# Kernel optimization log

Hardware: AMD Instinct MI355X
Metric: run time of the kernel (lower is better)

The kernel has to match this reference:

```python
import jax, jax.numpy as jnp
import numpy as np

WINDOW_SIZE = 11
C1 = 0.01 ** 2
C2 = 0.03 ** 2


def _make_window(size: int) -> jnp.ndarray:
    sigma = size / 6.0
    coords = jnp.arange(size, dtype=jnp.float32) - size // 2
    g = jnp.exp(-coords ** 2 / (2 * sigma ** 2))
    g = g / g.sum()
    w = jnp.outer(g, g)
    return w[None, None]  # [1,1,K,K]  (OIHW)


def _conv(x, w, pad):
    # x: [N,1,H,W], w: [1,1,K,K]
    return jax.lax.conv_general_dilated(
        x, w,
        window_strides=(1, 1),
        padding=[(pad, pad), (pad, pad)],
        dimension_numbers=("NCHW", "OIHW", "NCHW"),
    )


def setup_inputs() -> dict:
    key = jax.random.key(0)
    k1, k2 = jax.random.split(key)
    pred = jax.random.uniform(k1, (64, 1, 512, 512), dtype=jnp.float32)
    gt = jax.random.uniform(k2, (64, 1, 512, 512), dtype=jnp.float32)
    return {"pred": pred, "gt": gt}


def reference(pred, gt):
    w = _make_window(WINDOW_SIZE).astype(pred.dtype)
    pad = WINDOW_SIZE // 2
    mu1 = _conv(pred, w, pad)
    mu2 = _conv(gt, w, pad)
    sigma1 = _conv(pred * pred, w, pad) - mu1 ** 2
    sigma2 = _conv(gt * gt, w, pad) - mu2 ** 2
    sigma12 = _conv(pred * gt, w, pad) - mu1 * mu2
    ssim_map = (2 * mu1 * mu2 + C1) * (2 * sigma12 + C2) / (
        (mu1 ** 2 + mu2 ** 2 + C1) * (sigma1 + sigma2 + C2)
    )
    return 1 - ssim_map.mean()
```

## Files before the change

### kernel.cpp

```cpp
#include <hip/hip_runtime.h>
#include <math.h>
#include <type_traits>

#define IMG_H 512
#define IMG_W 512
#define NIMG 64
#define TH 64
#define HALO 5
#define KSIZE 11
#define LROW 74

__global__ __launch_bounds__(256, 4)
void ssim_main(const float* __restrict__ pred, const float* __restrict__ gt,
               float* __restrict__ partial) {
    __shared__ float sp[4][LROW];
    __shared__ float sg[4][LROW];
    __shared__ float wsum[4];

    const int tid  = threadIdx.x;
    const int wv   = tid >> 6;
    const int lane = tid & 63;
    const int bid  = blockIdx.x;
    const int img  = bid >> 4;
    const int rem  = bid & 15;
    const int c0   = (rem & 1) * 256 + wv * 64;
    const int r0   = (rem >> 1) * TH;

    float wgt[KSIZE];
    {
        const float sigma = 11.0f / 6.0f;
        float s = 0.f;
        #pragma unroll
        for (int i = 0; i < KSIZE; ++i) {
            float d = (float)(i - 5);
            wgt[i] = expf(-d * d / (2.f * sigma * sigma));
            s += wgt[i];
        }
        float inv = 1.f / s;
        #pragma unroll
        for (int i = 0; i < KSIZE; ++i) wgt[i] *= inv;
    }

    const float* pimg = pred + (size_t)img * IMG_H * IMG_W;
    const float* gimg = gt   + (size_t)img * IMG_H * IMG_W;

    const int  cs0  = c0 - HALO + lane;
    const int  cs1  = cs0 + 64;
    const bool has2 = lane < (LROW - 64);
    const bool c0ok = (cs0 >= 0) && (cs0 < IMG_W);
    const bool c1ok = has2 && (cs1 < IMG_W);
    const int  r_in0 = r0 - HALO;
    const int  rtop  = r_in0 + 73;

    float stp0, stp1, stg0, stg1;
    auto load_row = [&](int rr) {
        const bool rok = (rr >= 0) && (rr < IMG_H) && (rr <= rtop);
        const float* prow = pimg + (size_t)rr * IMG_W;
        const float* grow = gimg + (size_t)rr * IMG_W;
        stp0 = (rok && c0ok) ? prow[cs0] : 0.f;
        stg0 = (rok && c0ok) ? grow[cs0] : 0.f;
        stp1 = (rok && c1ok) ? prow[cs1] : 0.f;
        stg1 = (rok && c1ok) ? grow[cs1] : 0.f;
    };
    load_row(r_in0);

    float rp[KSIZE], rg[KSIZE], rpp[KSIZE], rgg[KSIZE], rpg[KSIZE];
    float lsum = 0.f;
    const float C1v = 1e-4f;
    const float C2v = 9e-4f;

    float* swp = &sp[wv][0];
    float* swg = &sg[wv][0];

    auto step = [&](int i, auto jc) {
        constexpr int jj = decltype(jc)::value;
        const int r = r_in0 + i;

        __builtin_amdgcn_wave_barrier();

        swp[lane] = stp0;
        swg[lane] = stg0;
        if (has2) { swp[lane + 64] = stp1; swg[lane + 64] = stg1; }

        load_row(r + 1);

        __builtin_amdgcn_wave_barrier();

        float hp = 0.f, hg = 0.f, hpp = 0.f, hgg = 0.f, hpg = 0.f;
        #pragma unroll
        for (int k = 0; k < KSIZE; ++k) {
            float p  = swp[lane + k];
            float g  = swg[lane + k];
            float t1 = wgt[k] * p;
            float t2 = wgt[k] * g;
            hp += t1;
            hg += t2;
            hpp = fmaf(t1, p, hpp);
            hgg = fmaf(t2, g, hgg);
            hpg = fmaf(t1, g, hpg);
        }
        rp[jj] = hp; rg[jj] = hg; rpp[jj] = hpp; rgg[jj] = hgg; rpg[jj] = hpg;

        if (i >= 10 && i < 10 + TH) {
            float mu1 = 0.f, mu2 = 0.f, svpp = 0.f, svgg = 0.f, svpg = 0.f;
            #pragma unroll
            for (int d = 0; d < KSIZE; ++d) {
                const int slot = (jj + 1 + d) % KSIZE;
                const float wv2 = wgt[d];
                mu1  = fmaf(wv2, rp[slot],  mu1);
                mu2  = fmaf(wv2, rg[slot],  mu2);
                svpp = fmaf(wv2, rpp[slot], svpp);
                svgg = fmaf(wv2, rgg[slot], svgg);
                svpg = fmaf(wv2, rpg[slot], svpg);
            }
            const float m11 = mu1 * mu1;
            const float m22 = mu2 * mu2;
            const float m12 = mu1 * mu2;
            const float s1  = svpp - m11;
            const float s2  = svgg - m22;
            const float s12 = svpg - m12;
            const float num = fmaf(2.f, m12, C1v) * fmaf(2.f, s12, C2v);
            const float den = (m11 + m22 + C1v) * (s1 + s2 + C2v);
            lsum += num * __builtin_amdgcn_rcpf(den);
        }
    };

    #pragma unroll 1
    for (int ob = 0; ob < 7; ++ob) {
        const int base = ob * KSIZE;
        step(base + 0,  std::integral_constant<int, 0>{});
        step(base + 1,  std::integral_constant<int, 1>{});
        step(base + 2,  std::integral_constant<int, 2>{});
        step(base + 3,  std::integral_constant<int, 3>{});
        step(base + 4,  std::integral_constant<int, 4>{});
        step(base + 5,  std::integral_constant<int, 5>{});
        step(base + 6,  std::integral_constant<int, 6>{});
        step(base + 7,  std::integral_constant<int, 7>{});
        step(base + 8,  std::integral_constant<int, 8>{});
        step(base + 9,  std::integral_constant<int, 9>{});
        step(base + 10, std::integral_constant<int, 10>{});
    }

    #pragma unroll
    for (int off = 32; off > 0; off >>= 1) lsum += __shfl_down(lsum, off);
    if (lane == 0) wsum[wv] = lsum;
    __syncthreads();
    if (tid == 0) {
        float b = wsum[0] + wsum[1] + wsum[2] + wsum[3];
        atomicAdd(partial, b);
    }
}

__global__ void ssim_final(const float* __restrict__ partial,
                           float* __restrict__ out) {
    out[0] = 1.f - partial[0] * (1.f / (float)((size_t)NIMG * IMG_H * IMG_W));
}

extern "C" void kernel_launch(void* const* d_in, const int* in_sizes, int n_in,
                              void* d_out, int out_size, void* d_ws, size_t ws_size,
                              hipStream_t stream) {
    const float* pred = (const float*)d_in[0];
    const float* gt   = (const float*)d_in[1];
    float* out = (float*)d_out;
    float* ws  = (float*)d_ws;

    hipMemsetAsync(ws, 0, sizeof(float), stream);

    const int nblocks = NIMG * 16;
    ssim_main<<<nblocks, 256, 0, stream>>>(pred, gt, ws);
    ssim_final<<<1, 1, 0, stream>>>(ws, out);
}
```

Before: 185.3 us.

## Halve row tile, fold symmetric Gaussian taps, interleave pred/gt in LDS

Reduces the row tile from 64 to 32 rows per wave, doubling the block count, and raises the launch-bounds occupancy hint. The horizontal pass now exploits the symmetric Gaussian to pair taps, and pred/gt are stored interleaved as float2 in shared memory so one LDS read fetches both. Weights become compile-time constants instead of being computed with expf. The trade-off is more halo rows loaded per output row.

```diff
diff --git a/kernel.cpp b/kernel.cpp
--- a/kernel.cpp
+++ b/kernel.cpp
@@ -5,44 +5,32 @@
 #define IMG_H 512
 #define IMG_W 512
 #define NIMG 64
-#define TH 64
+#define TH 32
 #define HALO 5
 #define KSIZE 11
 #define LROW 74
+#define NROWS (TH + 2*HALO)
 
-__global__ __launch_bounds__(256, 4)
+__global__ __launch_bounds__(256, 8)
 void ssim_main(const float* __restrict__ pred, const float* __restrict__ gt,
                float* __restrict__ partial) {
-    __shared__ float sp[4][LROW];
-    __shared__ float sg[4][LROW];
+    __shared__ float2 spg[4][LROW];
     __shared__ float wsum[4];
 
     const int tid  = threadIdx.x;
     const int wv   = tid >> 6;
     const int lane = tid & 63;
     const int bid  = blockIdx.x;
-    const int img  = bid >> 4;
-    const int rem  = bid & 15;
+    const int img  = bid >> 5;
+    const int rem  = bid & 31;
     const int c0   = (rem & 1) * 256 + wv * 64;
     const int r0   = (rem >> 1) * TH;
 
-    float wgt[KSIZE];
-    {
-        const float sigma = 11.0f / 6.0f;
-        float s = 0.f;
-        #pragma unroll
-        for (int i = 0; i < KSIZE; ++i) {
-            float d = (float)(i - 5);
-            wgt[i] = expf(-d * d / (2.f * sigma * sigma));
-            s += wgt[i];
-        }
-        float inv = 1.f / s;
-        #pragma unroll
-        for (int i = 0; i < KSIZE; ++i) wgt[i] *= inv;
-    }
+    constexpr float W[6] = {0.0052913f, 0.0201843f, 0.0571853f,
+                            0.1203038f, 0.1879737f, 0.2181237f};
 
-    const float* pimg = pred + (size_t)img * IMG_H * IMG_W;
-    const float* gimg = gt   + (size_t)img * IMG_H * IMG_W;
+    const float* pimg = pred + (size_t)img * (IMG_H * IMG_W);
+    const float* gimg = gt   + (size_t)img * (IMG_H * IMG_W);
 
     const int  cs0  = c0 - HALO + lane;
     const int  cs1  = cs0 + 64;
@@ -50,11 +38,11 @@
     const bool c0ok = (cs0 >= 0) && (cs0 < IMG_W);
     const bool c1ok = has2 && (cs1 < IMG_W);
     const int  r_in0 = r0 - HALO;
-    const int  rtop  = r_in0 + 73;
+    const int  rlast = r_in0 + NROWS - 1;
 
     float stp0, stp1, stg0, stg1;
     auto load_row = [&](int rr) {
-        const bool rok = (rr >= 0) && (rr < IMG_H) && (rr <= rtop);
+        const bool rok = (rr >= 0) && (rr < IMG_H) && (rr <= rlast);
         const float* prow = pimg + (size_t)rr * IMG_W;
         const float* grow = gimg + (size_t)rr * IMG_W;
         stp0 = (rok && c0ok) ? prow[cs0] : 0.f;
@@ -69,49 +57,49 @@
     const float C1v = 1e-4f;
     const float C2v = 9e-4f;
 
-    float* swp = &sp[wv][0];
-    float* swg = &sg[wv][0];
+    float2* sw = &spg[wv][0];
 
     auto step = [&](int i, auto jc) {
         constexpr int jj = decltype(jc)::value;
         const int r = r_in0 + i;
 
         __builtin_amdgcn_wave_barrier();
-
-        swp[lane] = stp0;
-        swg[lane] = stg0;
-        if (has2) { swp[lane + 64] = stp1; swg[lane + 64] = stg1; }
-
+        sw[lane] = make_float2(stp0, stg0);
+        if (has2) sw[lane + 64] = make_float2(stp1, stg1);
         load_row(r + 1);
-
         __builtin_amdgcn_wave_barrier();
 
-        float hp = 0.f, hg = 0.f, hpp = 0.f, hgg = 0.f, hpg = 0.f;
+        float2 vc = sw[lane + 5];
+        float t1 = W[5] * vc.x;
+        float t2 = W[5] * vc.y;
+        float hp = t1, hg = t2;
+        float hpp = t1 * vc.x;
+        float hgg = t2 * vc.y;
+        float hpg = t1 * vc.y;
         #pragma unroll
-        for (int k = 0; k < KSIZE; ++k) {
-            float p  = swp[lane + k];
-            float g  = swg[lane + k];
-            float t1 = wgt[k] * p;
-            float t2 = wgt[k] * g;
-            hp += t1;
-            hg += t2;
-            hpp = fmaf(t1, p, hpp);
-            hgg = fmaf(t2, g, hgg);
-            hpg = fmaf(t1, g, hpg);
+        for (int k = 0; k < 5; ++k) {
+            float2 vA = sw[lane + k];
+            float2 vB = sw[lane + 10 - k];
+            const float w = W[k];
+            hp  = fmaf(w, vA.x + vB.x, hp);
+            hg  = fmaf(w, vA.y + vB.y, hg);
+            hpp = fmaf(w, fmaf(vA.x, vA.x, vB.x * vB.x), hpp);
+            hgg = fmaf(w, fmaf(vA.y, vA.y, vB.y * vB.y), hgg);
+            hpg = fmaf(w, fmaf(vA.x, vA.y, vB.x * vB.y), hpg);
         }
         rp[jj] = hp; rg[jj] = hg; rpp[jj] = hpp; rgg[jj] = hgg; rpg[jj] = hpg;
 
-        if (i >= 10 && i < 10 + TH) {
+        if (i >= 10 && i < NROWS) {
             float mu1 = 0.f, mu2 = 0.f, svpp = 0.f, svgg = 0.f, svpg = 0.f;
             #pragma unroll
             for (int d = 0; d < KSIZE; ++d) {
                 const int slot = (jj + 1 + d) % KSIZE;
-                const float wv2 = wgt[d];
-                mu1  = fmaf(wv2, rp[slot],  mu1);
-                mu2  = fmaf(wv2, rg[slot],  mu2);
-                svpp = fmaf(wv2, rpp[slot], svpp);
-                svgg = fmaf(wv2, rgg[slot], svgg);
-                svpg = fmaf(wv2, rpg[slot], svpg);
+                const float w = W[d < 6 ? d : 10 - d];
+                mu1  = fmaf(w, rp[slot],  mu1);
+                mu2  = fmaf(w, rg[slot],  mu2);
+                svpp = fmaf(w, rpp[slot], svpp);
+                svgg = fmaf(w, rgg[slot], svgg);
+                svpg = fmaf(w, rpg[slot], svpg);
             }
             const float m11 = mu1 * mu1;
             const float m22 = mu2 * mu2;
@@ -125,21 +113,17 @@
         }
     };
 
+    #define S_(I, J) step((I), std::integral_constant<int, (J)>{})
     #pragma unroll 1
-    for (int ob = 0; ob < 7; ++ob) {
-        const int base = ob * KSIZE;
-        step(base + 0,  std::integral_constant<int, 0>{});
-        step(base + 1,  std::integral_constant<int, 1>{});
-        step(base + 2,  std::integral_constant<int, 2>{});
-        step(base + 3,  std::integral_constant<int, 3>{});
-        step(base + 4,  std::integral_constant<int, 4>{});
-        step(base + 5,  std::integral_constant<int, 5>{});
-        step(base + 6,  std::integral_constant<int, 6>{});
-        step(base + 7,  std::integral_constant<int, 7>{});
-        step(base + 8,  std::integral_constant<int, 8>{});
-        step(base + 9,  std::integral_constant<int, 9>{});
-        step(base + 10, std::integral_constant<int, 10>{});
+    for (int ob = 0; ob < 3; ++ob) {
+        const int b = ob * KSIZE;
+        S_(b + 0, 0);  S_(b + 1, 1);  S_(b + 2, 2);  S_(b + 3, 3);
+        S_(b + 4, 4);  S_(b + 5, 5);  S_(b + 6, 6);  S_(b + 7, 7);
+        S_(b + 8, 8);  S_(b + 9, 9);  S_(b + 10, 10);
     }
+    S_(33, 0); S_(34, 1); S_(35, 2); S_(36, 3); S_(37, 4);
+    S_(38, 5); S_(39, 6); S_(40, 7); S_(41, 8);
+    #undef S_
 
     #pragma unroll
     for (int off = 32; off > 0; off >>= 1) lsum += __shfl_down(lsum, off);
@@ -166,7 +150,7 @@
 
     hipMemsetAsync(ws, 0, sizeof(float), stream);
 
-    const int nblocks = NIMG * 16;
+    const int nblocks = NIMG * 32;
     ssim_main<<<nblocks, 256, 0, stream>>>(pred, gt, ws);
     ssim_final<<<1, 1, 0, stream>>>(ws, out);
 }
```

Result: slower. 589.5 us (+218.2%).
